# Optimization experiments

Measured on AMD Instinct MI355X. Metric: run time of the kernel, lower is better.

Reference implementation:

```python
import jax, jax.numpy as jnp
import numpy as np

N, E, G, D, L, EA = 100000, 1600000, 128, 128, 3, 7
BN_EPS = 1e-5


def _bn(x, g, b, m, v):
    # eval-mode BatchNorm1d with running stats
    return (x - m) * (g / jnp.sqrt(v + BN_EPS)) + b


def setup_inputs() -> dict:
    key = jax.random.key(0)
    ks = iter(jax.random.split(key, 64))
    nrm = lambda shape, s: jax.random.normal(next(ks), shape, jnp.float32) * s
    unif = lambda shape: jax.random.uniform(next(ks), shape, jnp.float32) * 0.5 + 0.5
    inp = {
        # forward tensor args
        'x': jnp.zeros((N,), jnp.int32),  # indices into Embedding(1, D) -> all zero
        'edge_index': jax.random.randint(next(ks), (2, E), 0, N, jnp.int32),
        'edge_attr': nrm((E, EA), 1.0),
        'batch': jnp.sort(jax.random.randint(next(ks), (N,), 0, G, jnp.int32)),
        # embeddings
        'node_emb': nrm((1, D), 1.0),
        'vn_emb': nrm((1, D), 0.1),
        # per-layer GINConv params (stacked on leading layer dim)
        'edge_W': nrm((L, EA, D), EA ** -0.5), 'edge_b': jnp.zeros((L, D), jnp.float32),
        'eps': jnp.zeros((L,), jnp.float32),
        'mlp_W1': nrm((L, D, 2 * D), D ** -0.5), 'mlp_b1': jnp.zeros((L, 2 * D), jnp.float32),
        'mbn_g': jnp.ones((L, 2 * D), jnp.float32), 'mbn_b': jnp.zeros((L, 2 * D), jnp.float32),
        'mbn_m': nrm((L, 2 * D), 0.1), 'mbn_v': unif((L, 2 * D)),
        'mlp_W2': nrm((L, 2 * D, D), (2 * D) ** -0.5), 'mlp_b2': jnp.zeros((L, D), jnp.float32),
        # outer per-layer BatchNorm
        'bn_g': jnp.ones((L, D), jnp.float32), 'bn_b': jnp.zeros((L, D), jnp.float32),
        'bn_m': nrm((L, D), 0.1), 'bn_v': unif((L, D)),
        # virtual-node MLPs (L-1 of them)
        'vn_W1': nrm((L - 1, D, 2 * D), D ** -0.5), 'vn_b1': jnp.zeros((L - 1, 2 * D), jnp.float32),
        'vbn1_g': jnp.ones((L - 1, 2 * D), jnp.float32), 'vbn1_b': jnp.zeros((L - 1, 2 * D), jnp.float32),
        'vbn1_m': nrm((L - 1, 2 * D), 0.1), 'vbn1_v': unif((L - 1, 2 * D)),
        'vn_W2': nrm((L - 1, 2 * D, D), (2 * D) ** -0.5), 'vn_b2': jnp.zeros((L - 1, D), jnp.float32),
        'vbn2_g': jnp.ones((L - 1, D), jnp.float32), 'vbn2_b': jnp.zeros((L - 1, D), jnp.float32),
        'vbn2_m': nrm((L - 1, D), 0.1), 'vbn2_v': unif((L - 1, D)),
    }
    return inp


def reference(x, edge_index, edge_attr, batch, node_emb, vn_emb,
              edge_W, edge_b, eps, mlp_W1, mlp_b1, mbn_g, mbn_b, mbn_m, mbn_v,
              mlp_W2, mlp_b2, bn_g, bn_b, bn_m, bn_v,
              vn_W1, vn_b1, vbn1_g, vbn1_b, vbn1_m, vbn1_v,
              vn_W2, vn_b2, vbn2_g, vbn2_b, vbn2_m, vbn2_v):
    src, dst = edge_index[0], edge_index[1]
    h = node_emb[x]                                # [N, D] node encoder gather
    vn = jnp.broadcast_to(vn_emb[0], (G, D))       # virtual node per graph
    for l in range(L):
        h_in = h + vn[batch]                       # broadcast virtual node to nodes
        # GINConv
        e = edge_attr @ edge_W[l] + edge_b[l]      # [E, D]
        msg = jax.nn.relu(h_in[src] + e)           # gather + edge fuse
        agg = jax.ops.segment_sum(msg, dst, num_segments=N)
        z = (1.0 + eps[l]) * h_in + agg
        z = jax.nn.relu(_bn(z @ mlp_W1[l] + mlp_b1[l], mbn_g[l], mbn_b[l], mbn_m[l], mbn_v[l]))
        h2 = z @ mlp_W2[l] + mlp_b2[l]
        # outer BatchNorm (+ relu except last layer; dropout is identity in eval)
        h2 = _bn(h2, bn_g[l], bn_b[l], bn_m[l], bn_v[l])
        h = h2 if l == L - 1 else jax.nn.relu(h2)
        if l < L - 1:
            vt = jax.ops.segment_sum(h_in, batch, num_segments=G) + vn  # global_add_pool
            t = jax.nn.relu(_bn(vt @ vn_W1[l] + vn_b1[l], vbn1_g[l], vbn1_b[l], vbn1_m[l], vbn1_v[l]))
            vn = jax.nn.relu(_bn(t @ vn_W2[l] + vn_b2[l], vbn2_g[l], vbn2_b[l], vbn2_m[l], vbn2_v[l]))
    return h  # JK == 'last'
```

## Files before the change

kernel.cpp:

```cpp
#include <hip/hip_runtime.h>
#include <hip/hip_bf16.h>

#define NN 100000
#define NP 100032
#define EE 1600000
#define GG 128
#define DD 128
#define LL 3
#define EAA 7
#define BN_EPS 1e-5f

typedef __attribute__((ext_vector_type(8))) short bf16x8;
typedef __attribute__((ext_vector_type(4))) float f32x4;
typedef __attribute__((ext_vector_type(4))) unsigned short u16x4;

__device__ __forceinline__ unsigned short f2bf(float x) {
    unsigned int u = __float_as_uint(x);
    u = (u + 0x7FFF + ((u >> 16) & 1)) >> 16;
    return (unsigned short)u;
}
__device__ __forceinline__ float bf2f(unsigned short h) {
    return __uint_as_float(((unsigned int)h) << 16);
}
__device__ __forceinline__ float bflo(unsigned int u) {
    return __uint_as_float(u << 16);
}
__device__ __forceinline__ float bfhi(unsigned int u) {
    return __uint_as_float(u & 0xFFFF0000u);
}

__global__ __launch_bounds__(256) void init_kernel(
    const int* __restrict__ x, const float* __restrict__ node_emb,
    const float* __restrict__ vn_emb, float* __restrict__ h,
    float* __restrict__ vn)
{
    long i = (long)blockIdx.x * 256 + threadIdx.x;
    if (i < (long)NN * DD) {
        int node = (int)(i >> 7), d = (int)(i & 127);
        h[i] = node_emb[(long)x[node] * DD + d];
    }
    if (i < GG * DD) vn[i] = vn_emb[i & 127];
}

#define R1 8
__global__ __launch_bounds__(256) void hin_kernel(
    float* __restrict__ hbuf,
    unsigned short* __restrict__ h16,
    const float* __restrict__ vn,
    const int* __restrict__ batch,
    const float* __restrict__ eps,
    float* __restrict__ agg,
    float* __restrict__ vt,
    int layer, int accum_vt, int write_agg)
{
    const int d  = threadIdx.x & 127;
    const int rg = threadIdx.x >> 7;
    const float epl = 1.0f + eps[layer];
    const long row0 = (long)blockIdx.x * (R1 * 2);

    float vacc = 0.0f;
    int   vb   = -1;
    #pragma unroll
    for (int r = 0; r < R1; ++r) {
        long row = row0 + rg + 2 * r;
        if (row >= NN) break;
        int b = batch[row];
        long idx = row * DD + d;
        float hv = hbuf[idx] + vn[(long)b * DD + d];
        hbuf[idx] = hv;
        h16[idx]  = f2bf(hv);
        if (write_agg) agg[idx] = epl * hv;
        if (accum_vt) {
            if (b != vb) {
                if (vb >= 0) atomicAdd(&vt[(long)vb * DD + d], vacc);
                vb = b; vacc = 0.0f;
            }
            vacc += hv;
        }
    }
    if (accum_vt && vb >= 0) atomicAdd(&vt[(long)vb * DD + d], vacc);
}

__global__ __launch_bounds__(256) void count_kernel(
    const int* __restrict__ ei, int* __restrict__ deg)
{
    long e = (long)blockIdx.x * 256 + threadIdx.x;
    if (e < EE) atomicAdd(&deg[ei[EE + e]], 1);
}

__global__ __launch_bounds__(1024) void scan_a(
    const int* __restrict__ deg, int* __restrict__ rp, int* __restrict__ partials)
{
    __shared__ int s[1024];
    int t = threadIdx.x;
    long i = (long)blockIdx.x * 1024 + t;
    int v = (i < NN) ? deg[i] : 0;
    s[t] = v;
    __syncthreads();
    for (int off = 1; off < 1024; off <<= 1) {
        int u = (t >= off) ? s[t - off] : 0;
        __syncthreads();
        s[t] += u;
        __syncthreads();
    }
    if (i < NN) rp[i] = s[t] - v;
    if (t == 1023) partials[blockIdx.x] = s[1023];
}

__global__ void scan_b(int* __restrict__ partials, int nb)
{
    if (threadIdx.x == 0) {
        int run = 0;
        for (int i = 0; i < nb; ++i) { int v = partials[i]; partials[i] = run; run += v; }
    }
}

__global__ __launch_bounds__(1024) void scan_c(
    int* __restrict__ rp, int* __restrict__ fill, const int* __restrict__ partials)
{
    long i = (long)blockIdx.x * 1024 + threadIdx.x;
    if (i < NN) {
        int v = rp[i] + partials[blockIdx.x];
        rp[i] = v;
        fill[i] = v;
    }
    if (i == 0) rp[NN] = EE;
}

__global__ __launch_bounds__(256) void scatter_kernel(
    const int* __restrict__ ei, const float* __restrict__ eattr,
    int* __restrict__ fill, unsigned short* __restrict__ attr16,
    int* __restrict__ src_arr, int* __restrict__ eid_perm)
{
    long e = (long)blockIdx.x * 256 + threadIdx.x;
    if (e >= EE) return;
    int dst = ei[EE + e];
    int pos = atomicAdd(&fill[dst], 1);
    if (attr16) {
        u16x4 w0, w1;
        w0.x = f2bf(eattr[e * EAA + 0]);
        w0.y = f2bf(eattr[e * EAA + 1]);
        w0.z = f2bf(eattr[e * EAA + 2]);
        w0.w = f2bf(eattr[e * EAA + 3]);
        w1.x = f2bf(eattr[e * EAA + 4]);
        w1.y = f2bf(eattr[e * EAA + 5]);
        w1.z = f2bf(eattr[e * EAA + 6]);
        w1.w = 0;
        *(u16x4*)(attr16 + (long)pos * 8)     = w0;
        *(u16x4*)(attr16 + (long)pos * 8 + 4) = w1;
        src_arr[pos] = ei[e];
    } else {
        eid_perm[pos] = (int)e;
    }
}

__global__ __launch_bounds__(256) void gin_agg_kernel(
    const float* __restrict__ h_in,
    const unsigned short* __restrict__ h16,
    const int* __restrict__ rp,
    const unsigned short* __restrict__ attr16,
    const int* __restrict__ src_arr,
    const float* __restrict__ eW, const float* __restrict__ eb,
    const float* __restrict__ eps,
    float* __restrict__ agg, int layer)
{
    const int lane = threadIdx.x & 63;
    const int wid  = threadIdx.x >> 6;
    const long n   = (long)blockIdx.x * 4 + wid;
    const int d0   = lane * 2;

    const float* eWl = eW + (long)layer * EAA * DD;
    float2 w2[EAA];
    #pragma unroll
    for (int a = 0; a < EAA; ++a)
        w2[a] = *(const float2*)&eWl[a * DD + d0];
    const float2 bias = *(const float2*)&eb[layer * DD + d0];
    const float  epl  = 1.0f + eps[layer];

    float2 hn = *(const float2*)&h_in[n * DD + d0];
    float accx = epl * hn.x, accy = epl * hn.y;

    int p  = rp[n];
    const int p1 = rp[n + 1];

    #define EDGE(AU, GU)                                                      \
    {                                                                         \
        float a0 = bflo(AU.x), a1 = bfhi(AU.x);                               \
        float a2 = bflo(AU.y), a3 = bfhi(AU.y);                               \
        float a4 = bflo(AU.z), a5 = bfhi(AU.z);                               \
        float a6 = bflo(AU.w);                                                \
        float ex = bias.x, ey = bias.y;                                       \
        ex = fmaf(a0, w2[0].x, ex); ey = fmaf(a0, w2[0].y, ey);               \
        ex = fmaf(a1, w2[1].x, ex); ey = fmaf(a1, w2[1].y, ey);               \
        ex = fmaf(a2, w2[2].x, ex); ey = fmaf(a2, w2[2].y, ey);               \
        ex = fmaf(a3, w2[3].x, ex); ey = fmaf(a3, w2[3].y, ey);               \
        ex = fmaf(a4, w2[4].x, ex); ey = fmaf(a4, w2[4].y, ey);               \
        ex = fmaf(a5, w2[5].x, ex); ey = fmaf(a5, w2[5].y, ey);               \
        ex = fmaf(a6, w2[6].x, ex); ey = fmaf(a6, w2[6].y, ey);               \
        float mx = bflo(GU) + ex, my = bfhi(GU) + ey;                         \
        accx += fmaxf(mx, 0.0f); accy += fmaxf(my, 0.0f);                     \
    }

    for (; p + 4 <= p1; p += 4) {
        int s0 = src_arr[p];
        int s1 = src_arr[p + 1];
        int s2 = src_arr[p + 2];
        int s3 = src_arr[p + 3];
        const uint4* a4p = (const uint4*)(attr16 + (long)p * 8);
        uint4 A0 = a4p[0];
        uint4 A1 = a4p[1];
        uint4 A2 = a4p[2];
        uint4 A3 = a4p[3];
        unsigned int g0 = *(const unsigned int*)(h16 + (long)s0 * DD + d0);
        unsigned int g1 = *(const unsigned int*)(h16 + (long)s1 * DD + d0);
        unsigned int g2 = *(const unsigned int*)(h16 + (long)s2 * DD + d0);
        unsigned int g3 = *(const unsigned int*)(h16 + (long)s3 * DD + d0);
        EDGE(A0, g0)
        EDGE(A1, g1)
        EDGE(A2, g2)
        EDGE(A3, g3)
    }
    for (; p < p1; ++p) {
        int s = src_arr[p];
        uint4 A = *(const uint4*)(attr16 + (long)p * 8);
        unsigned int g = *(const unsigned int*)(h16 + (long)s * DD + d0);
        EDGE(A, g)
    }
    #undef EDGE

    *(float2*)&agg[n * DD + d0] = make_float2(accx, accy);
}

__global__ __launch_bounds__(256) void gin_agg_eid_kernel(
    const float* __restrict__ h_in,
    const int* __restrict__ rp,
    const int* __restrict__ eid_perm,
    const int* __restrict__ ei,
    const float* __restrict__ eattr,
    const float* __restrict__ eW, const float* __restrict__ eb,
    const float* __restrict__ eps,
    float* __restrict__ agg, int layer)
{
    const int d    = threadIdx.x & 127;
    const int half = threadIdx.x >> 7;
    const long n   = (long)blockIdx.x * 2 + half;

    float w[EAA];
    #pragma unroll
    for (int a = 0; a < EAA; ++a) w[a] = eW[layer * EAA * DD + a * DD + d];
    const float bias = eb[layer * DD + d];
    const float epl  = 1.0f + eps[layer];

    float acc = epl * h_in[n * DD + d];
    const int p0 = rp[n], p1 = rp[n + 1];
    for (int p = p0; p < p1; ++p) {
        int e = eid_perm[p];
        int src = ei[e];
        float ea = bias;
        #pragma unroll
        for (int a = 0; a < EAA; ++a)
            ea = fmaf(eattr[(long)e * EAA + a], w[a], ea);
        float m = h_in[(long)src * DD + d] + ea;
        acc += m > 0.0f ? m : 0.0f;
    }
    agg[n * DD + d] = acc;
}

#define EPB 64
__global__ __launch_bounds__(256) void edge_kernel(
    const float* __restrict__ h_in,
    const int* __restrict__ ei,
    const float* __restrict__ eattr,
    const float* __restrict__ eW,
    const float* __restrict__ eb,
    float* __restrict__ agg,
    int layer)
{
    const int d    = threadIdx.x & 127;
    const int esub = threadIdx.x >> 7;
    float w[EAA];
    #pragma unroll
    for (int a = 0; a < EAA; ++a) w[a] = eW[layer * EAA * DD + a * DD + d];
    const float bias = eb[layer * DD + d];

    const long base = (long)blockIdx.x * EPB;
    for (int k = esub; k < EPB; k += 2) {
        long e = base + k;
        if (e >= EE) break;
        int s = ei[e];
        int t = ei[EE + e];
        float acc = bias;
        #pragma unroll
        for (int a = 0; a < EAA; ++a)
            acc = fmaf(eattr[e * EAA + a], w[a], acc);
        float m = h_in[(long)s * DD + d] + acc;
        m = m > 0.0f ? m : 0.0f;
        atomicAdd(&agg[(long)t * DD + d], m);
    }
}

__global__ __launch_bounds__(256) void wprep_kernel(
    const float* __restrict__ W1, const float* __restrict__ W2,
    unsigned short* __restrict__ w1h, unsigned short* __restrict__ w1l,
    unsigned short* __restrict__ w2h, unsigned short* __restrict__ w2l)
{
    int tid = blockIdx.x * 256 + threadIdx.x;
    if (tid >= LL * 2 * 32768) return;
    int l = tid / 65536;
    int rem = tid - l * 65536;
    int mat = rem >> 15;
    int fi = rem & 32767;
    int b = fi & 7, lane = (fi >> 3) & 63;
    int kgrp = ((lane >> 4) << 3) + b;
    if (mat == 0) {
        int mt = (fi >> 9) & 15, kk = fi >> 13;
        int m = (mt << 4) + (lane & 15);
        int k = (kk << 5) + kgrp;
        float v = W1[(long)l * DD * 2 * DD + (long)k * 2 * DD + m];
        unsigned short hi = f2bf(v);
        w1h[(long)l * 32768 + fi] = hi;
        w1l[(long)l * 32768 + fi] = f2bf(v - bf2f(hi));
    } else {
        int mt = (fi >> 9) & 7, kk = fi >> 12;
        int m = (mt << 4) + (lane & 15);
        int k = (kk << 5) + kgrp;
        float v = W2[(long)l * 2 * DD * DD + (long)k * DD + m];
        unsigned short hi = f2bf(v);
        w2h[(long)l * 32768 + fi] = hi;
        w2l[(long)l * 32768 + fi] = f2bf(v - bf2f(hi));
    }
}

__global__ __launch_bounds__(256) void bnprep_kernel(
    const float* __restrict__ b1, const float* __restrict__ g1,
    const float* __restrict__ be1, const float* __restrict__ m1,
    const float* __restrict__ v1,
    const float* __restrict__ b2, const float* __restrict__ g2,
    const float* __restrict__ be2, const float* __restrict__ m2,
    const float* __restrict__ v2,
    float* __restrict__ sc1, float* __restrict__ sh1,
    float* __restrict__ sc2, float* __restrict__ sh2)
{
    int tid = blockIdx.x * 256 + threadIdx.x;
    if (tid < LL * 2 * DD) {
        float sc = g1[tid] / sqrtf(v1[tid] + BN_EPS);
        sc1[tid] = sc;
        sh1[tid] = (b1[tid] - m1[tid]) * sc + be1[tid];
    }
    int t2 = tid - LL * 2 * DD;
    if (t2 >= 0 && t2 < LL * DD) {
        float sc = g2[t2] / sqrtf(v2[t2] + BN_EPS);
        sc2[t2] = sc;
        sh2[t2] = (b2[t2] - m2[t2]) * sc + be2[t2];
    }
}

__global__ __launch_bounds__(256, 2) void mlp_mfma_kernel(
    const float* __restrict__ z_in,
    const unsigned short* __restrict__ w1h, const unsigned short* __restrict__ w1l,
    const unsigned short* __restrict__ w2h, const unsigned short* __restrict__ w2l,
    const float* __restrict__ sc1, const float* __restrict__ sh1,
    const float* __restrict__ sc2, const float* __restrict__ sh2,
    float* __restrict__ h_out, int layer, int do_relu)
{
    __shared__ char lds[65536];
    const int tid  = threadIdx.x;
    const int lane = tid & 63;
    const int wv   = tid >> 6;
    const long row0 = (long)blockIdx.x * 64;
    const int kb = (lane >> 4) << 3;

    {
        const float4* zi = (const float4*)(z_in + row0 * DD);
        #pragma unroll
        for (int i = 0; i < 8; ++i) {
            int idx = tid + i * 256;
            float4 v = zi[idx];
            int r = idx >> 5;
            int c = (idx & 31) << 2;
            u16x4 hv, lv;
            hv.x = f2bf(v.x); lv.x = f2bf(v.x - bf2f(hv.x));
            hv.y = f2bf(v.y); lv.y = f2bf(v.y - bf2f(hv.y));
            hv.z = f2bf(v.z); lv.z = f2bf(v.z - bf2f(hv.z));
            hv.w = f2bf(v.w); lv.w = f2bf(v.w - bf2f(hv.w));
            int off = ((r << 8) + (c << 1)) ^ ((r & 7) << 4);
            *(u16x4*)(lds + off)         = hv;
            *(u16x4*)(lds + 16384 + off) = lv;
        }
    }
    __syncthreads();

    bf16x8 B1h[4][4], B1l[4][4];
    #pragma unroll
    for (int nt = 0; nt < 4; ++nt) {
        int r = (nt << 4) + (lane & 15);
        #pragma unroll
        for (int kk = 0; kk < 4; ++kk) {
            int off = ((r << 8) + (((kk << 5) + kb) << 1)) ^ ((r & 7) << 4);
            B1h[nt][kk] = *(const bf16x8*)(lds + off);
            B1l[nt][kk] = *(const bf16x8*)(lds + 16384 + off);
        }
    }
    __syncthreads();

    const unsigned short* w1hl = w1h + (long)layer * 32768;
    const unsigned short* w1ll = w1l + (long)layer * 32768;
    #pragma unroll
    for (int mtl = 0; mtl < 4; ++mtl) {
        const int mt = (wv << 2) + mtl;
        bf16x8 Ah[4], Al[4];
        #pragma unroll
        for (int kk = 0; kk < 4; ++kk) {
            const long boff = ((long)((kk << 4) + mt) * 64 + lane) << 3;
            Ah[kk] = *(const bf16x8*)(w1hl + boff);
            Al[kk] = *(const bf16x8*)(w1ll + boff);
        }
        f32x4 acc[4];
        #pragma unroll
        for (int nt = 0; nt < 4; ++nt) acc[nt] = (f32x4){0.f, 0.f, 0.f, 0.f};
        #pragma unroll
        for (int kk = 0; kk < 4; ++kk) {
            #pragma unroll
            for (int nt = 0; nt < 4; ++nt) {
                acc[nt] = __builtin_amdgcn_mfma_f32_16x16x32_bf16(Ah[kk], B1h[nt][kk], acc[nt], 0, 0, 0);
                acc[nt] = __builtin_amdgcn_mfma_f32_16x16x32_bf16(Ah[kk], B1l[nt][kk], acc[nt], 0, 0, 0);
                acc[nt] = __builtin_amdgcn_mfma_f32_16x16x32_bf16(Al[kk], B1h[nt][kk], acc[nt], 0, 0, 0);
            }
        }
        const int m0 = (mt << 4) + ((lane >> 4) << 2);
        const float4 s4 = *(const float4*)&sc1[layer * 2 * DD + m0];
        const float4 t4 = *(const float4*)&sh1[layer * 2 * DD + m0];
        #pragma unroll
        for (int nt = 0; nt < 4; ++nt) {
            int row = (nt << 4) + (lane & 15);
            float u0 = fmaxf(fmaf(acc[nt][0], s4.x, t4.x), 0.0f);
            float u1 = fmaxf(fmaf(acc[nt][1], s4.y, t4.y), 0.0f);
            float u2 = fmaxf(fmaf(acc[nt][2], s4.z, t4.z), 0.0f);
            float u3 = fmaxf(fmaf(acc[nt][3], s4.w, t4.w), 0.0f);
            u16x4 hv, lv;
            hv.x = f2bf(u0); lv.x = f2bf(u0 - bf2f(hv.x));
            hv.y = f2bf(u1); lv.y = f2bf(u1 - bf2f(hv.y));
            hv.z = f2bf(u2); lv.z = f2bf(u2 - bf2f(hv.z));
            hv.w = f2bf(u3); lv.w = f2bf(u3 - bf2f(hv.w));
            int off = ((row << 9) + (m0 << 1)) ^ ((row & 7) << 4);
            *(u16x4*)(lds + off)         = hv;
            *(u16x4*)(lds + 32768 + off) = lv;
        }
    }
    __syncthreads();

    const unsigned short* w2hl = w2h + (long)layer * 32768;
    const unsigned short* w2ll = w2l + (long)layer * 32768;
    f32x4 acc2[2][4];
    #pragma unroll
    for (int mtl = 0; mtl < 2; ++mtl)
        #pragma unroll
        for (int nt = 0; nt < 4; ++nt) acc2[mtl][nt] = (f32x4){0.f, 0.f, 0.f, 0.f};

    #pragma unroll
    for (int kk = 0; kk < 8; ++kk) {
        bf16x8 Bh[4], Bl[4];
        #pragma unroll
        for (int nt = 0; nt < 4; ++nt) {
            int r = (nt << 4) + (lane & 15);
            int off = ((r << 9) + (((kk << 5) + kb) << 1)) ^ ((r & 7) << 4);
            Bh[nt] = *(const bf16x8*)(lds + off);
            Bl[nt] = *(const bf16x8*)(lds + 32768 + off);
        }
        #pragma unroll
        for (int mtl = 0; mtl < 2; ++mtl) {
            const int mt = (wv << 1) + mtl;
            const long boff = ((long)((kk << 3) + mt) * 64 + lane) << 3;
            bf16x8 Ah = *(const bf16x8*)(w2hl + boff);
            bf16x8 Al = *(const bf16x8*)(w2ll + boff);
            #pragma unroll
            for (int nt = 0; nt < 4; ++nt) {
                acc2[mtl][nt] = __builtin_amdgcn_mfma_f32_16x16x32_bf16(Ah, Bh[nt], acc2[mtl][nt], 0, 0, 0);
                acc2[mtl][nt] = __builtin_amdgcn_mfma_f32_16x16x32_bf16(Ah, Bl[nt], acc2[mtl][nt], 0, 0, 0);
                acc2[mtl][nt] = __builtin_amdgcn_mfma_f32_16x16x32_bf16(Al, Bh[nt], acc2[mtl][nt], 0, 0, 0);
            }
        }
    }
    #pragma unroll
    for (int mtl = 0; mtl < 2; ++mtl) {
        const int m0 = ((((wv << 1) + mtl)) << 4) + ((lane >> 4) << 2);
        const float4 s4 = *(const float4*)&sc2[layer * DD + m0];
        const float4 t4 = *(const float4*)&sh2[layer * DD + m0];
        #pragma unroll
        for (int nt = 0; nt < 4; ++nt) {
            long row = row0 + (nt << 4) + (lane & 15);
            if (row < NN) {
                float4 o;
                o.x = fmaf(acc2[mtl][nt][0], s4.x, t4.x);
                o.y = fmaf(acc2[mtl][nt][1], s4.y, t4.y);
                o.z = fmaf(acc2[mtl][nt][2], s4.z, t4.z);
                o.w = fmaf(acc2[mtl][nt][3], s4.w, t4.w);
                if (do_relu) {
                    o.x = fmaxf(o.x, 0.0f); o.y = fmaxf(o.y, 0.0f);
                    o.z = fmaxf(o.z, 0.0f); o.w = fmaxf(o.w, 0.0f);
                }
                *(float4*)&h_out[row * DD + m0] = o;
            }
        }
    }
}

__global__ __launch_bounds__(256) void vn_kernel(
    const float* __restrict__ vt, float* __restrict__ vn,
    const float* __restrict__ W1, const float* __restrict__ b1,
    const float* __restrict__ g1, const float* __restrict__ be1,
    const float* __restrict__ m1, const float* __restrict__ v1,
    const float* __restrict__ W2, const float* __restrict__ b2,
    const float* __restrict__ g2, const float* __restrict__ be2,
    const float* __restrict__ m2, const float* __restrict__ v2,
    int layer)
{
    __shared__ float row[DD];
    __shared__ float u[2 * DD];
    const int g = blockIdx.x;
    const int t = threadIdx.x;

    if (t < DD) row[t] = vt[(long)g * DD + t] + vn[(long)g * DD + t];
    __syncthreads();

    {
        const float* W = W1 + (long)layer * DD * 2 * DD;
        float acc = 0.0f;
        for (int k = 0; k < DD; ++k) acc = fmaf(row[k], W[k * 2 * DD + t], acc);
        const long o = (long)layer * 2 * DD + t;
        float sc = g1[o] / sqrtf(v1[o] + BN_EPS);
        float sh = be1[o] - m1[o] * sc;
        float val = (acc + b1[o]) * sc + sh;
        u[t] = val > 0.0f ? val : 0.0f;
    }
    __syncthreads();

    if (t < DD) {
        const float* W = W2 + (long)layer * 2 * DD * DD;
        float acc = 0.0f;
        for (int k = 0; k < 2 * DD; ++k) acc = fmaf(u[k], W[k * DD + t], acc);
        const long o = (long)layer * DD + t;
        float sc = g2[o] / sqrtf(v2[o] + BN_EPS);
        float sh = be2[o] - m2[o] * sc;
        float val = (acc + b2[o]) * sc + sh;
        vn[(long)g * DD + t] = val > 0.0f ? val : 0.0f;
    }
}

extern "C" void kernel_launch(void* const* d_in, const int* in_sizes, int n_in,
                              void* d_out, int out_size, void* d_ws, size_t ws_size,
                              hipStream_t stream)
{
    const int*   x       = (const int*)  d_in[0];
    const int*   ei      = (const int*)  d_in[1];
    const float* eattr   = (const float*)d_in[2];
    const int*   batch   = (const int*)  d_in[3];
    const float* node_emb= (const float*)d_in[4];
    const float* vn_emb  = (const float*)d_in[5];
    const float* edge_W  = (const float*)d_in[6];
    const float* edge_b  = (const float*)d_in[7];
    const float* eps     = (const float*)d_in[8];
    const float* mlp_W1  = (const float*)d_in[9];
    const float* mlp_b1  = (const float*)d_in[10];
    const float* mbn_g   = (const float*)d_in[11];
    const float* mbn_b   = (const float*)d_in[12];
    const float* mbn_m   = (const float*)d_in[13];
    const float* mbn_v   = (const float*)d_in[14];
    const float* mlp_W2  = (const float*)d_in[15];
    const float* mlp_b2  = (const float*)d_in[16];
    const float* bn_g    = (const float*)d_in[17];
    const float* bn_b    = (const float*)d_in[18];
    const float* bn_m    = (const float*)d_in[19];
    const float* bn_v    = (const float*)d_in[20];
    const float* vn_W1   = (const float*)d_in[21];
    const float* vn_b1   = (const float*)d_in[22];
    const float* vbn1_g  = (const float*)d_in[23];
    const float* vbn1_b  = (const float*)d_in[24];
    const float* vbn1_m  = (const float*)d_in[25];
    const float* vbn1_v  = (const float*)d_in[26];
    const float* vn_W2   = (const float*)d_in[27];
    const float* vn_b2   = (const float*)d_in[28];
    const float* vbn2_g  = (const float*)d_in[29];
    const float* vbn2_b  = (const float*)d_in[30];
    const float* vbn2_m  = (const float*)d_in[31];
    const float* vbn2_v  = (const float*)d_in[32];

    float* h = (float*)d_out;
    char*  ws = (char*)d_ws;

    size_t off = 0;
    auto alloc = [&](size_t bytes) -> void* {
        void* p = ws + off;
        off += (bytes + 255) & ~(size_t)255;
        return p;
    };
    const size_t GDB = (size_t)GG * DD * sizeof(float);

    float* agg      = (float*)alloc((size_t)NP * DD * sizeof(float));
    unsigned short* h16 = (unsigned short*)alloc((size_t)NN * DD * sizeof(unsigned short));
    float* vn       = (float*)alloc(GDB);
    float* vt       = (float*)alloc(GDB);
    int*   rp       = (int*)  alloc((NN + 1) * sizeof(int));
    int*   fill     = (int*)  alloc(NN * sizeof(int));
    int*   partials = (int*)  alloc(128 * sizeof(int));
    int*   src_arr  = (int*)  alloc((size_t)EE * sizeof(int));
    unsigned short* w1h = (unsigned short*)alloc(LL * 32768 * sizeof(unsigned short));
    unsigned short* w1l = (unsigned short*)alloc(LL * 32768 * sizeof(unsigned short));
    unsigned short* w2h = (unsigned short*)alloc(LL * 32768 * sizeof(unsigned short));
    unsigned short* w2l = (unsigned short*)alloc(LL * 32768 * sizeof(unsigned short));
    float* bn1sc = (float*)alloc(LL * 2 * DD * sizeof(float));
    float* bn1sh = (float*)alloc(LL * 2 * DD * sizeof(float));
    float* bn2sc = (float*)alloc(LL * DD * sizeof(float));
    float* bn2sh = (float*)alloc(LL * DD * sizeof(float));
    const size_t base_end = off;

    unsigned short* attr16 = nullptr;
    int* eid_perm = nullptr;
    if (ws_size >= base_end + (size_t)EE * 8 * sizeof(unsigned short))
        attr16 = (unsigned short*)alloc((size_t)EE * 8 * sizeof(unsigned short));
    else if (ws_size >= base_end + (size_t)EE * sizeof(int))
        eid_perm = (int*)alloc((size_t)EE * sizeof(int));
    const bool csr = (attr16 != nullptr) || (eid_perm != nullptr);

    {
        long total = (long)NN * DD;
        init_kernel<<<(int)((total + 255) / 256), 256, 0, stream>>>(
            x, node_emb, vn_emb, h, vn);
    }

    wprep_kernel<<<(LL * 2 * 32768 + 255) / 256, 256, 0, stream>>>(
        mlp_W1, mlp_W2, w1h, w1l, w2h, w2l);
    bnprep_kernel<<<(LL * 2 * DD + LL * DD + 255) / 256, 256, 0, stream>>>(
        mlp_b1, mbn_g, mbn_b, mbn_m, mbn_v,
        mlp_b2, bn_g, bn_b, bn_m, bn_v,
        bn1sc, bn1sh, bn2sc, bn2sh);

    if (csr) {
        const int egrid = (EE + 255) / 256;
        const int ngrid = (NN + 1023) / 1024;
        hipMemsetAsync(fill, 0, NN * sizeof(int), stream);
        count_kernel<<<egrid, 256, 0, stream>>>(ei, fill);
        scan_a<<<ngrid, 1024, 0, stream>>>(fill, rp, partials);
        scan_b<<<1, 64, 0, stream>>>(partials, ngrid);
        scan_c<<<ngrid, 1024, 0, stream>>>(rp, fill, partials);
        scatter_kernel<<<egrid, 256, 0, stream>>>(ei, eattr, fill, attr16, src_arr, eid_perm);
    }

    for (int l = 0; l < LL; ++l) {
        int accum = (l < LL - 1) ? 1 : 0;
        if (accum)
            hipMemsetAsync(vt, 0, GDB, stream);

        hin_kernel<<<NN / (R1 * 2), 256, 0, stream>>>(
            h, h16, vn, batch, eps, agg, vt, l, accum, csr ? 0 : 1);

        if (attr16) {
            gin_agg_kernel<<<NN / 4, 256, 0, stream>>>(
                h, h16, rp, attr16, src_arr, edge_W, edge_b, eps, agg, l);
        } else if (eid_perm) {
            gin_agg_eid_kernel<<<NN / 2, 256, 0, stream>>>(
                h, rp, eid_perm, ei, eattr, edge_W, edge_b, eps, agg, l);
        } else {
            edge_kernel<<<(EE + EPB - 1) / EPB, 256, 0, stream>>>(
                h, ei, eattr, edge_W, edge_b, agg, l);
        }

        mlp_mfma_kernel<<<NP / 64, 256, 0, stream>>>(
            agg, w1h, w1l, w2h, w2l, bn1sc, bn1sh, bn2sc, bn2sh,
            h, l, accum);

        if (accum)
            vn_kernel<<<GG, 256, 0, stream>>>(
                vt, vn, vn_W1, vn_b1, vbn1_g, vbn1_b, vbn1_m, vbn1_v,
                vn_W2, vn_b2, vbn2_g, vbn2_b, vbn2_m, vbn2_v, l);
    }
}
```

Baseline: 801.4 us.

## Specialize layer zero for constant node embedding and fuse virtual-node add into MLP epilogue

Since the node encoder has a single row, every node's layer-0 input is node_emb + vn_emb. Layer 0 therefore skips the init and h_in kernels and the per-edge source gather. Its pooled virtual-node sum is computed from per-graph node counts. For later layers, the next layer's h_in (h + vn[batch]) and its bf16 copy are produced in the MLP epilogue, with a separate small kernel for the pooled sum. This removes several full N×D passes and launches, at the cost of more specialized code paths that depend on the embedding table having one row.

```diff
diff --git a/kernel.cpp b/kernel.cpp
--- a/kernel.cpp
+++ b/kernel.cpp
@@ -79,6 +79,46 @@
         }
     }
     if (accum_vt && vb >= 0) atomicAdd(&vt[(long)vb * DD + d], vacc);
+}
+
+__global__ __launch_bounds__(256) void vt_kernel(
+    const float* __restrict__ hbuf, const int* __restrict__ batch,
+    float* __restrict__ vt)
+{
+    const int d  = threadIdx.x & 127;
+    const int rg = threadIdx.x >> 7;
+    const long row0 = (long)blockIdx.x * 16;
+    float vacc = 0.0f;
+    int   vb   = -1;
+    #pragma unroll
+    for (int r = 0; r < 8; ++r) {
+        long row = row0 + rg + 2 * r;
+        if (row >= NN) break;
+        int b = batch[row];
+        float hv = hbuf[row * DD + d];
+        if (b != vb) {
+            if (vb >= 0) atomicAdd(&vt[(long)vb * DD + d], vacc);
+            vb = b; vacc = 0.0f;
+        }
+        vacc += hv;
+    }
+    if (vb >= 0) atomicAdd(&vt[(long)vb * DD + d], vacc);
+}
+
+__global__ __launch_bounds__(256) void cnt_kernel(
+    const int* __restrict__ batch, int* __restrict__ cnt)
+{
+    const int tid = blockIdx.x * 256 + threadIdx.x;
+    const int CH  = (NN + 16383) / 16384;
+    long s = (long)tid * CH;
+    long e = s + CH; if (e > NN) e = NN;
+    int vb = -1, c = 0;
+    for (long i = s; i < e; ++i) {
+        int b = batch[i];
+        if (b != vb) { if (vb >= 0) atomicAdd(&cnt[vb], c); vb = b; c = 0; }
+        ++c;
+    }
+    if (vb >= 0) atomicAdd(&cnt[vb], c);
 }
 
 __global__ __launch_bounds__(256) void count_kernel(
@@ -152,6 +192,72 @@
     } else {
         eid_perm[pos] = (int)e;
     }
+}
+
+__global__ __launch_bounds__(256) void gin0_kernel(
+    const float* __restrict__ node_emb,
+    const float* __restrict__ vn_emb,
+    const int* __restrict__ rp,
+    const unsigned short* __restrict__ attr16,
+    const float* __restrict__ eW, const float* __restrict__ eb,
+    const float* __restrict__ eps,
+    float* __restrict__ agg)
+{
+    const int lane = threadIdx.x & 63;
+    const int wid  = threadIdx.x >> 6;
+    const long n   = (long)blockIdx.x * 4 + wid;
+    const int d0   = lane * 2;
+
+    float2 w2[EAA];
+    #pragma unroll
+    for (int a = 0; a < EAA; ++a)
+        w2[a] = *(const float2*)&eW[a * DD + d0];
+    const float2 bias = *(const float2*)&eb[d0];
+    const float  epl  = 1.0f + eps[0];
+
+    const float cx = node_emb[d0]     + vn_emb[d0];
+    const float cy = node_emb[d0 + 1] + vn_emb[d0 + 1];
+    float accx = epl * cx, accy = epl * cy;
+
+    int p  = rp[n];
+    const int p1 = rp[n + 1];
+
+    #define EDGE0(AU)                                                         \
+    {                                                                         \
+        float a0 = bflo(AU.x), a1 = bfhi(AU.x);                               \
+        float a2 = bflo(AU.y), a3 = bfhi(AU.y);                               \
+        float a4 = bflo(AU.z), a5 = bfhi(AU.z);                               \
+        float a6 = bflo(AU.w);                                                \
+        float ex = bias.x, ey = bias.y;                                       \
+        ex = fmaf(a0, w2[0].x, ex); ey = fmaf(a0, w2[0].y, ey);               \
+        ex = fmaf(a1, w2[1].x, ex); ey = fmaf(a1, w2[1].y, ey);               \
+        ex = fmaf(a2, w2[2].x, ex); ey = fmaf(a2, w2[2].y, ey);               \
+        ex = fmaf(a3, w2[3].x, ex); ey = fmaf(a3, w2[3].y, ey);               \
+        ex = fmaf(a4, w2[4].x, ex); ey = fmaf(a4, w2[4].y, ey);               \
+        ex = fmaf(a5, w2[5].x, ex); ey = fmaf(a5, w2[5].y, ey);               \
+        ex = fmaf(a6, w2[6].x, ex); ey = fmaf(a6, w2[6].y, ey);               \
+        float mx = cx + ex, my = cy + ey;                                     \
+        accx += fmaxf(mx, 0.0f); accy += fmaxf(my, 0.0f);                     \
+    }
+
+    for (; p + 4 <= p1; p += 4) {
+        const uint4* a4p = (const uint4*)(attr16 + (long)p * 8);
+        uint4 A0 = a4p[0];
+        uint4 A1 = a4p[1];
+        uint4 A2 = a4p[2];
+        uint4 A3 = a4p[3];
+        EDGE0(A0)
+        EDGE0(A1)
+        EDGE0(A2)
+        EDGE0(A3)
+    }
+    for (; p < p1; ++p) {
+        uint4 A = *(const uint4*)(attr16 + (long)p * 8);
+        EDGE0(A)
+    }
+    #undef EDGE0
+
+    *(float2*)&agg[n * DD + d0] = make_float2(accx, accy);
 }
 
 __global__ __launch_bounds__(256) void gin_agg_kernel(
@@ -361,7 +467,9 @@
     const unsigned short* __restrict__ w2h, const unsigned short* __restrict__ w2l,
     const float* __restrict__ sc1, const float* __restrict__ sh1,
     const float* __restrict__ sc2, const float* __restrict__ sh2,
-    float* __restrict__ h_out, int layer, int do_relu)
+    float* __restrict__ h_out, int layer, int do_relu,
+    const int* __restrict__ batch, const float* __restrict__ vnbuf,
+    unsigned short* __restrict__ h16, int fuse)
 {
     __shared__ char lds[65536];
     const int tid  = threadIdx.x;
@@ -490,16 +598,24 @@
         for (int nt = 0; nt < 4; ++nt) {
             long row = row0 + (nt << 4) + (lane & 15);
             if (row < NN) {
-                float4 o;
-                o.x = fmaf(acc2[mtl][nt][0], s4.x, t4.x);
-                o.y = fmaf(acc2[mtl][nt][1], s4.y, t4.y);
-                o.z = fmaf(acc2[mtl][nt][2], s4.z, t4.z);
-                o.w = fmaf(acc2[mtl][nt][3], s4.w, t4.w);
+                float o0 = fmaf(acc2[mtl][nt][0], s4.x, t4.x);
+                float o1 = fmaf(acc2[mtl][nt][1], s4.y, t4.y);
+                float o2 = fmaf(acc2[mtl][nt][2], s4.z, t4.z);
+                float o3 = fmaf(acc2[mtl][nt][3], s4.w, t4.w);
                 if (do_relu) {
-                    o.x = fmaxf(o.x, 0.0f); o.y = fmaxf(o.y, 0.0f);
-                    o.z = fmaxf(o.z, 0.0f); o.w = fmaxf(o.w, 0.0f);
+                    o0 = fmaxf(o0, 0.0f); o1 = fmaxf(o1, 0.0f);
+                    o2 = fmaxf(o2, 0.0f); o3 = fmaxf(o3, 0.0f);
                 }
-                *(float4*)&h_out[row * DD + m0] = o;
+                if (fuse) {
+                    int b = batch[row];
+                    float4 vnv = *(const float4*)&vnbuf[(long)b * DD + m0];
+                    o0 += vnv.x; o1 += vnv.y; o2 += vnv.z; o3 += vnv.w;
+                    u16x4 hv;
+                    hv.x = f2bf(o0); hv.y = f2bf(o1);
+                    hv.z = f2bf(o2); hv.w = f2bf(o3);
+                    *(u16x4*)&h16[row * DD + m0] = hv;
+                }
+                *(float4*)&h_out[row * DD + m0] = make_float4(o0, o1, o2, o3);
             }
         }
     }
@@ -543,6 +659,48 @@
         float sc = g2[o] / sqrtf(v2[o] + BN_EPS);
         float sh = be2[o] - m2[o] * sc;
         float val = (acc + b2[o]) * sc + sh;
+        vn[(long)g * DD + t] = val > 0.0f ? val : 0.0f;
+    }
+}
+
+__global__ __launch_bounds__(256) void vn0_kernel(
+    const int* __restrict__ cnt,
+    const float* __restrict__ node_emb, const float* __restrict__ vn_emb,
+    float* __restrict__ vn,
+    const float* __restrict__ W1, const float* __restrict__ b1,
+    const float* __restrict__ g1, const float* __restrict__ be1,
+    const float* __restrict__ m1, const float* __restrict__ v1,
+    const float* __restrict__ W2, const float* __restrict__ b2,
+    const float* __restrict__ g2, const float* __restrict__ be2,
+    const float* __restrict__ m2, const float* __restrict__ v2)
+{
+    __shared__ float row[DD];
+    __shared__ float u[2 * DD];
+    const int g = blockIdx.x;
+    const int t = threadIdx.x;
+
+    if (t < DD) {
+        float c = node_emb[t] + vn_emb[t];
+        row[t] = (float)cnt[g] * c + vn_emb[t];
+    }
+    __syncthreads();
+
+    {
+        float acc = 0.0f;
+        for (int k = 0; k < DD; ++k) acc = fmaf(row[k], W1[k * 2 * DD + t], acc);
+        float sc = g1[t] / sqrtf(v1[t] + BN_EPS);
+        float sh = be1[t] - m1[t] * sc;
+        float val = (acc + b1[t]) * sc + sh;
+        u[t] = val > 0.0f ? val : 0.0f;
+    }
+    __syncthreads();
+
+    if (t < DD) {
+        float acc = 0.0f;
+        for (int k = 0; k < 2 * DD; ++k) acc = fmaf(u[k], W2[k * DD + t], acc);
+        float sc = g2[t] / sqrtf(v2[t] + BN_EPS);
+        float sh = be2[t] - m2[t] * sc;
+        float val = (acc + b2[t]) * sc + sh;
         vn[(long)g * DD + t] = val > 0.0f ? val : 0.0f;
     }
 }
@@ -603,6 +761,7 @@
     int*   rp       = (int*)  alloc((NN + 1) * sizeof(int));
     int*   fill     = (int*)  alloc(NN * sizeof(int));
     int*   partials = (int*)  alloc(128 * sizeof(int));
+    int*   cnt      = (int*)  alloc(GG * sizeof(int));
     int*   src_arr  = (int*)  alloc((size_t)EE * sizeof(int));
     unsigned short* w1h = (unsigned short*)alloc(LL * 32768 * sizeof(unsigned short));
     unsigned short* w1l = (unsigned short*)alloc(LL * 32768 * sizeof(unsigned short));
@@ -620,13 +779,6 @@
         attr16 = (unsigned short*)alloc((size_t)EE * 8 * sizeof(unsigned short));
     else if (ws_size >= base_end + (size_t)EE * sizeof(int))
         eid_perm = (int*)alloc((size_t)EE * sizeof(int));
-    const bool csr = (attr16 != nullptr) || (eid_perm != nullptr);
-
-    {
-        long total = (long)NN * DD;
-        init_kernel<<<(int)((total + 255) / 256), 256, 0, stream>>>(
-            x, node_emb, vn_emb, h, vn);
-    }
 
     wprep_kernel<<<(LL * 2 * 32768 + 255) / 256, 256, 0, stream>>>(
         mlp_W1, mlp_W2, w1h, w1l, w2h, w2l);
@@ -635,6 +787,7 @@
         mlp_b2, bn_g, bn_b, bn_m, bn_v,
         bn1sc, bn1sh, bn2sc, bn2sh);
 
+    const bool csr = (attr16 != nullptr) || (eid_perm != nullptr);
     if (csr) {
         const int egrid = (EE + 255) / 256;
         const int ngrid = (NN + 1023) / 1024;
@@ -646,32 +799,66 @@
         scatter_kernel<<<egrid, 256, 0, stream>>>(ei, eattr, fill, attr16, src_arr, eid_perm);
     }
 
-    for (int l = 0; l < LL; ++l) {
-        int accum = (l < LL - 1) ? 1 : 0;
-        if (accum)
-            hipMemsetAsync(vt, 0, GDB, stream);
-
-        hin_kernel<<<NN / (R1 * 2), 256, 0, stream>>>(
-            h, h16, vn, batch, eps, agg, vt, l, accum, csr ? 0 : 1);
-
-        if (attr16) {
-            gin_agg_kernel<<<NN / 4, 256, 0, stream>>>(
-                h, h16, rp, attr16, src_arr, edge_W, edge_b, eps, agg, l);
-        } else if (eid_perm) {
-            gin_agg_eid_kernel<<<NN / 2, 256, 0, stream>>>(
-                h, rp, eid_perm, ei, eattr, edge_W, edge_b, eps, agg, l);
-        } else {
-            edge_kernel<<<(EE + EPB - 1) / EPB, 256, 0, stream>>>(
-                h, ei, eattr, edge_W, edge_b, agg, l);
-        }
-
+    if (attr16) {
+        hipMemsetAsync(cnt, 0, GG * sizeof(int), stream);
+        cnt_kernel<<<64, 256, 0, stream>>>(batch, cnt);
+
+        vn0_kernel<<<GG, 256, 0, stream>>>(
+            cnt, node_emb, vn_emb, vn,
+            vn_W1, vn_b1, vbn1_g, vbn1_b, vbn1_m, vbn1_v,
+            vn_W2, vn_b2, vbn2_g, vbn2_b, vbn2_m, vbn2_v);
+        gin0_kernel<<<NN / 4, 256, 0, stream>>>(
+            node_emb, vn_emb, rp, attr16, edge_W, edge_b, eps, agg);
         mlp_mfma_kernel<<<NP / 64, 256, 0, stream>>>(
             agg, w1h, w1l, w2h, w2l, bn1sc, bn1sh, bn2sc, bn2sh,
-            h, l, accum);
-
-        if (accum)
-            vn_kernel<<<GG, 256, 0, stream>>>(
-                vt, vn, vn_W1, vn_b1, vbn1_g, vbn1_b, vbn1_m, vbn1_v,
-                vn_W2, vn_b2, vbn2_g, vbn2_b, vbn2_m, vbn2_v, l);
-    }
-}
+            h, 0, 1, batch, vn, h16, 1);
+
+        hipMemsetAsync(vt, 0, GDB, stream);
+        vt_kernel<<<NN / 16, 256, 0, stream>>>(h, batch, vt);
+        vn_kernel<<<GG, 256, 0, stream>>>(
+            vt, vn, vn_W1, vn_b1, vbn1_g, vbn1_b, vbn1_m, vbn1_v,
+            vn_W2, vn_b2, vbn2_g, vbn2_b, vbn2_m, vbn2_v, 1);
+        gin_agg_kernel<<<NN / 4, 256, 0, stream>>>(
+            h, h16, rp, attr16, src_arr, edge_W, edge_b, eps, agg, 1);
+        mlp_mfma_kernel<<<NP / 64, 256, 0, stream>>>(
+            agg, w1h, w1l, w2h, w2l, bn1sc, bn1sh, bn2sc, bn2sh,
+            h, 1, 1, batch, vn, h16, 1);
+
+        gin_agg_kernel<<<NN / 4, 256, 0, stream>>>(
+            h, h16, rp, attr16, src_arr, edge_W, edge_b, eps, agg, 2);
+        mlp_mfma_kernel<<<NP / 64, 256, 0, stream>>>(
+            agg, w1h, w1l, w2h, w2l, bn1sc, bn1sh, bn2sc, bn2sh,
+            h, 2, 0, batch, vn, h16, 0);
+    } else {
+        {
+            long total = (long)NN * DD;
+            init_kernel<<<(int)((total + 255) / 256), 256, 0, stream>>>(
+                x, node_emb, vn_emb, h, vn);
+        }
+        for (int l = 0; l < LL; ++l) {
+            int accum = (l < LL - 1) ? 1 : 0;
+            if (accum)
+                hipMemsetAsync(vt, 0, GDB, stream);
+
+            hin_kernel<<<NN / (R1 * 2), 256, 0, stream>>>(
+                h, h16, vn, batch, eps, agg, vt, l, accum, csr ? 0 : 1);
+
+            if (eid_perm) {
+                gin_agg_eid_kernel<<<NN / 2, 256, 0, stream>>>(
+                    h, rp, eid_perm, ei, eattr, edge_W, edge_b, eps, agg, l);
+            } else {
+                edge_kernel<<<(EE + EPB - 1) / EPB, 256, 0, stream>>>(
+                    h, ei, eattr, edge_W, edge_b, agg, l);
+            }
+
+            mlp_mfma_kernel<<<NP / 64, 256, 0, stream>>>(
+                agg, w1h, w1l, w2h, w2l, bn1sc, bn1sh, bn2sc, bn2sh,
+                h, l, accum, batch, vn, h16, 0);
+
+            if (accum)
+                vn_kernel<<<GG, 256, 0, stream>>>(
+                    vt, vn, vn_W1, vn_b1, vbn1_g, vbn1_b, vbn1_m, vbn1_v,
+                    vn_W2, vn_b2, vbn2_g, vbn2_b, vbn2_m, vbn2_v, l);
+        }
+    }
+}
```

Measured after the change: 766.9 us. 1.04x faster.
